# Kernel tuning notes

Measured on AMD Instinct MI355X. Metric: run time of the kernel, lower is better.

Reference implementation:

```python
import jax, jax.numpy as jnp
import numpy as np

Q_MAX = 127.0  # int8 symmetric quant range


def setup_inputs() -> dict:
    key = jax.random.key(0)
    kx, kw, ks = jax.random.split(key, 3)
    M, K, N = 16384, 4096, 4096
    x = jax.random.normal(kx, (M, K), dtype=jnp.float32)
    # int8 weight values in [-127, 127]
    weight = jax.random.randint(kw, (N, K), -127, 128, dtype=jnp.int32).astype(jnp.int8)
    # per-output-row dequant scale, small positive values as a real quantizer would produce
    weight_scale = jax.random.uniform(ks, (N, 1), dtype=jnp.float32, minval=1e-3, maxval=1e-2)
    return {"x": x, "weight": weight, "weight_scale": weight_scale}


def reference(x, weight, weight_scale):
    # --- per-token dynamic activation quantization (get_hip_quant(per_Token)) ---
    amax = jnp.max(jnp.abs(x), axis=-1, keepdims=True)            # [M,1]
    x_scale = amax / Q_MAX                                        # [M,1]
    x_q = jnp.clip(jnp.round(x / jnp.maximum(x_scale, 1e-8)), -Q_MAX, Q_MAX)  # int8 values, kept fp32
    # --- gemm_a8w8: int8xint8 GEMM with fused dequant (row scale_a * col scale_b) ---
    acc = jnp.einsum('mk,nk->mn', x_q, weight.astype(jnp.float32),
                     preferred_element_type=jnp.float32)          # [M,N] int accumulation in fp32
    y = acc * x_scale * weight_scale.T                            # fused dequant scales
    return y  # fp32 stand-in for otype=bf16 output
```

## Files before the change

### kernel.cpp

```cpp
#include <hip/hip_runtime.h>
#include <stdint.h>

#define M_DIM 16384
#define N_DIM 4096
#define K_DIM 4096

#define BM 256
#define BN 256
#define BK 128
#define NT (K_DIM / BK)

typedef int i32x4 __attribute__((ext_vector_type(4)));

__device__ __forceinline__ void async16(const uint8_t* g, uint8_t* l) {
    __builtin_amdgcn_global_load_lds(
        (const __attribute__((address_space(1))) void*)g,
        (__attribute__((address_space(3))) void*)l,
        16, 0, 0);
}

__global__ __launch_bounds__(256) void pack_w_kernel(const int* __restrict__ w32,
                                                     uint32_t* __restrict__ w8,
                                                     int n4) {
    int i = blockIdx.x * 256 + threadIdx.x;
    if (i < n4) {
        const int4 v = reinterpret_cast<const int4*>(w32)[i];
        uint32_t p = (uint32_t)(v.x & 255) | ((uint32_t)(v.y & 255) << 8) |
                     ((uint32_t)(v.z & 255) << 16) | ((uint32_t)(v.w & 255) << 24);
        w8[i] = p;
    }
}

__global__ __launch_bounds__(256) void quant_kernel(const float* __restrict__ x,
                                                    uint32_t* __restrict__ xq,
                                                    float* __restrict__ xscale) {
    const int m = blockIdx.x;
    const int t = threadIdx.x;
    const float4* row = reinterpret_cast<const float4*>(x + (size_t)m * K_DIM);
    float4 v[4];
    float amax = 0.0f;
#pragma unroll
    for (int i = 0; i < 4; ++i) {
        v[i] = row[t + i * 256];
        amax = fmaxf(amax, fmaxf(fmaxf(fabsf(v[i].x), fabsf(v[i].y)),
                                 fmaxf(fabsf(v[i].z), fabsf(v[i].w))));
    }
#pragma unroll
    for (int off = 32; off > 0; off >>= 1) amax = fmaxf(amax, __shfl_xor(amax, off));
    __shared__ float smax[4];
    if ((t & 63) == 0) smax[t >> 6] = amax;
    __syncthreads();
    amax = fmaxf(fmaxf(smax[0], smax[1]), fmaxf(smax[2], smax[3]));
    const float scale = amax / 127.0f;
    const float s = fmaxf(scale, 1e-8f);
    if (t == 0) xscale[m] = scale;
    uint32_t* orow = xq + (size_t)m * (K_DIM / 4);
#pragma unroll
    for (int i = 0; i < 4; ++i) {
        int q0 = __float2int_rn(v[i].x / s);
        int q1 = __float2int_rn(v[i].y / s);
        int q2 = __float2int_rn(v[i].z / s);
        int q3 = __float2int_rn(v[i].w / s);
        q0 = max(-127, min(127, q0));
        q1 = max(-127, min(127, q1));
        q2 = max(-127, min(127, q2));
        q3 = max(-127, min(127, q3));
        uint32_t p = (uint32_t)(q0 & 255) | ((uint32_t)(q1 & 255) << 8) |
                     ((uint32_t)(q2 & 255) << 16) | ((uint32_t)(q3 & 255) << 24);
        orow[t + i * 256] = p;
    }
}

__global__ __launch_bounds__(512, 2) void gemm_kernel(
    const uint8_t* __restrict__ Aq, const float* __restrict__ ascale,
    const uint8_t* __restrict__ Bq, const float* __restrict__ wscale,
    float* __restrict__ out) {
    __shared__ uint8_t lds[4 * BM * BK];
    uint8_t* ldsA0 = lds;
    uint8_t* ldsA1 = lds + BM * BK;
    uint8_t* ldsB0 = lds + 2 * BM * BK;
    uint8_t* ldsB1 = lds + 3 * BM * BK;

    const int tid = threadIdx.x;
    const int lane = tid & 63;
    const int w = tid >> 6;
    const int wr = w >> 2;
    const int wc = w & 3;
    const int lr = lane & 15;
    const int lg = lane >> 4;

    const int bid = blockIdx.x;
    const int swz = (bid & 7) * (1024 / 8) + (bid >> 3);
    const size_t row0 = (size_t)(swz >> 4) * BM;
    const size_t col0 = (size_t)(swz & 15) * BN;
    const uint8_t* Ab = Aq + row0 * K_DIM;
    const uint8_t* Bb = Bq + col0 * K_DIM;

    i32x4 acc[8][4];
#pragma unroll
    for (int i = 0; i < 8; ++i)
#pragma unroll
        for (int j = 0; j < 4; ++j) acc[i][j] = (i32x4){0, 0, 0, 0};

#define STAGE_P(BASE, DST, KT)                                                   \
    do {                                                                         \
        _Pragma("unroll") for (int it_ = 0; it_ < 4; ++it_) {                    \
            const int idx_ = it_ * 512 + tid;                                    \
            const int m_ = idx_ >> 3, p_ = idx_ & 7;                             \
            async16((BASE) + (size_t)m_ * K_DIM + (KT) * BK +                    \
                        ((p_ ^ (m_ & 7)) << 4),                                  \
                    (DST) + (it_ * 512 + w * 64) * 16);                          \
        }                                                                        \
    } while (0)

#define READ_K(BUFA, BUFB, KK, F)                                                \
    do {                                                                         \
        _Pragma("unroll") for (int q_ = 0; q_ < 8; ++q_) {                       \
            const int r_ = wr * 128 + q_ * 16 + lr;                              \
            const int u_ = (KK) * 4 + lg;                                        \
            afk[F][q_] = *reinterpret_cast<const i32x4*>(                        \
                (BUFA) + r_ * BK + ((u_ ^ (r_ & 7)) << 4));                      \
        }                                                                        \
        _Pragma("unroll") for (int p_ = 0; p_ < 4; ++p_) {                       \
            const int r_ = wc * 64 + p_ * 16 + lr;                               \
            const int u_ = (KK) * 4 + lg;                                        \
            bfk[F][p_] = *reinterpret_cast<const i32x4*>(                        \
                (BUFB) + r_ * BK + ((u_ ^ (r_ & 7)) << 4));                      \
        }                                                                        \
    } while (0)

#define CLUSTER(F)                                                               \
    do {                                                                         \
        __builtin_amdgcn_s_setprio(1);                                           \
        _Pragma("unroll") for (int q_ = 0; q_ < 8; ++q_)                         \
        _Pragma("unroll") for (int p_ = 0; p_ < 4; ++p_)                         \
            acc[q_][p_] = __builtin_amdgcn_mfma_i32_16x16x64_i8(                 \
                afk[F][q_], bfk[F][p_], acc[q_][p_], 0, 0, 0);                   \
        __builtin_amdgcn_s_setprio(0);                                           \
    } while (0)

#define BAR __builtin_amdgcn_s_barrier()
#define VMCNT(N) asm volatile("s_waitcnt vmcnt(" #N ")" ::: "memory")
#define LGKM0                                              \
    do {                                                   \
        asm volatile("s_waitcnt lgkmcnt(0)" ::: "memory"); \
        __builtin_amdgcn_sched_barrier(0);                 \
    } while (0)

#define TILE_ONE(CA, CB, NA, NB, TB, TA2, KA, KB)                                \
    do {                                                                         \
        LGKM0;                                               \
        STAGE_P(Bb, NB, TB);               \
        READ_K(CA, CB, KB, 1);           \
        CLUSTER(0);                                                              \
        LGKM0;                                                     \
        VMCNT(0);                     \
        BAR;                           \
        STAGE_P(Ab, CA, TA2);               \
        READ_K(NA, NB, KA, 0);            \
        CLUSTER(1);                                                              \
    } while (0)

#define MAIN_LOOP(KA, KB)                                                        \
    do {                                                                         \
        READ_K(ldsA0, ldsB0, KA, 0);                                             \
        _Pragma("unroll 1") for (int it2 = 0; it2 < NT / 2; ++it2) {             \
            const int T = 2 * it2;                                               \
            const int Tp2 = (T + 2 < NT) ? T + 2 : NT - 1;                       \
            const int Tp3 = (T + 3 < NT) ? T + 3 : NT - 1;                       \
            TILE_ONE(ldsA0, ldsB0, ldsA1, ldsB1, T + 1, Tp2, KA, KB);            \
            TILE_ONE(ldsA1, ldsB1, ldsA0, ldsB0, Tp2, Tp3, KA, KB);              \
        }                                                                        \
    } while (0)

    i32x4 afk[2][8], bfk[2][4];

    STAGE_P(Ab, ldsA0, 0);
    STAGE_P(Bb, ldsB0, 0);
    STAGE_P(Ab, ldsA1, 1);
    VMCNT(4);
    BAR;

    if (wr == 0) {
        MAIN_LOOP(0, 1);
    } else {
        MAIN_LOOP(1, 0);
    }

    const float* asp = ascale + row0 + wr * 128;
    const float* wsp = wscale + col0 + wc * 64;
    float wsv[4];
#pragma unroll
    for (int nf = 0; nf < 4; ++nf) wsv[nf] = wsp[nf * 16 + lr];
    float* outBase = out + (row0 + wr * 128) * (size_t)N_DIM + col0 + wc * 64;
#pragma unroll
    for (int mf = 0; mf < 8; ++mf) {
#pragma unroll
        for (int j = 0; j < 4; ++j) {
            const int r = mf * 16 + lg * 4 + j;
            const float av = asp[r];
            float* orow = outBase + (size_t)r * N_DIM;
#pragma unroll
            for (int nf = 0; nf < 4; ++nf) {
                orow[nf * 16 + lr] = (float)acc[mf][nf][j] * av * wsv[nf];
            }
        }
    }
#undef STAGE_P
#undef READ_K
#undef CLUSTER
#undef TILE_ONE
#undef MAIN_LOOP
#undef BAR
#undef VMCNT
#undef LGKM0
}

extern "C" void kernel_launch(void* const* d_in, const int* in_sizes, int n_in,
                              void* d_out, int out_size, void* d_ws, size_t ws_size,
                              hipStream_t stream) {
    const float* x = (const float*)d_in[0];
    const int* w32 = (const int*)d_in[1];
    const float* wscale = (const float*)d_in[2];
    float* out = (float*)d_out;

    uint8_t* ws = (uint8_t*)d_ws;
    uint32_t* xq = (uint32_t*)ws;
    float* xscale = (float*)(ws + (size_t)M_DIM * K_DIM);
    uint8_t* wq = ws + (size_t)M_DIM * K_DIM + (size_t)M_DIM * 4;

    pack_w_kernel<<<dim3((N_DIM * K_DIM / 4 + 255) / 256), 256, 0, stream>>>(
        w32, (uint32_t*)wq, N_DIM * K_DIM / 4);
    quant_kernel<<<dim3(M_DIM), 256, 0, stream>>>(x, xq, xscale);
    gemm_kernel<<<dim3((M_DIM / BM) * (N_DIM / BN)), 512, 0, stream>>>(
        (const uint8_t*)xq, xscale, wq, wscale, out);
}
```

Baseline: 343.8 us.

## Merge prep kernels, precompute LDS/global offsets, and unify GEMM staging schedule

Combines the weight-packing and activation-quantization kernels into a single launch, with extra blocks handling the weight pack. In the GEMM it precomputes the swizzled global and LDS offsets once per thread instead of per tile. It also replaces the per-wave-row split K-order main loop with a single loop that prefetches both A and B tiles two ahead, staging both after the barrier. This aims to cut address arithmetic and launch overhead, at the cost of more live registers and less staggered LDS traffic between wave rows.

```diff
diff --git a/kernel.cpp b/kernel.cpp
--- a/kernel.cpp
+++ b/kernel.cpp
@@ -19,23 +19,21 @@
         16, 0, 0);
 }
 
-__global__ __launch_bounds__(256) void pack_w_kernel(const int* __restrict__ w32,
-                                                     uint32_t* __restrict__ w8,
-                                                     int n4) {
-    int i = blockIdx.x * 256 + threadIdx.x;
-    if (i < n4) {
+__global__ __launch_bounds__(256) void prep_kernel(const float* __restrict__ x,
+                                                   const int* __restrict__ w32,
+                                                   uint32_t* __restrict__ xq,
+                                                   float* __restrict__ xscale,
+                                                   uint32_t* __restrict__ w8) {
+    const int b = blockIdx.x;
+    const int t = threadIdx.x;
+    if (b >= M_DIM) {
+        const int i = (b - M_DIM) * 256 + t;
         const int4 v = reinterpret_cast<const int4*>(w32)[i];
-        uint32_t p = (uint32_t)(v.x & 255) | ((uint32_t)(v.y & 255) << 8) |
-                     ((uint32_t)(v.z & 255) << 16) | ((uint32_t)(v.w & 255) << 24);
-        w8[i] = p;
-    }
-}
-
-__global__ __launch_bounds__(256) void quant_kernel(const float* __restrict__ x,
-                                                    uint32_t* __restrict__ xq,
-                                                    float* __restrict__ xscale) {
-    const int m = blockIdx.x;
-    const int t = threadIdx.x;
+        w8[i] = (uint32_t)(v.x & 255) | ((uint32_t)(v.y & 255) << 8) |
+                ((uint32_t)(v.z & 255) << 16) | ((uint32_t)(v.w & 255) << 24);
+        return;
+    }
+    const int m = b;
     const float4* row = reinterpret_cast<const float4*>(x + (size_t)m * K_DIM);
     float4 v[4];
     float amax = 0.0f;
@@ -65,9 +63,8 @@
         q1 = max(-127, min(127, q1));
         q2 = max(-127, min(127, q2));
         q3 = max(-127, min(127, q3));
-        uint32_t p = (uint32_t)(q0 & 255) | ((uint32_t)(q1 & 255) << 8) |
-                     ((uint32_t)(q2 & 255) << 16) | ((uint32_t)(q3 & 255) << 24);
-        orow[t + i * 256] = p;
+        orow[t + i * 256] = (uint32_t)(q0 & 255) | ((uint32_t)(q1 & 255) << 8) |
+                            ((uint32_t)(q2 & 255) << 16) | ((uint32_t)(q3 & 255) << 24);
     }
 }
 
@@ -96,37 +93,51 @@
     const uint8_t* Ab = Aq + row0 * K_DIM;
     const uint8_t* Bb = Bq + col0 * K_DIM;
 
+    int sgOff[4];
+#pragma unroll
+    for (int it = 0; it < 4; ++it) {
+        const int idx = it * 512 + tid;
+        const int m_ = idx >> 3, p_ = idx & 7;
+        sgOff[it] = m_ * K_DIM + ((p_ ^ (m_ & 7)) << 4);
+    }
+    int slOff[4];
+#pragma unroll
+    for (int it = 0; it < 4; ++it) slOff[it] = (it * 512 + w * 64) * 16;
+    int aRd[2][8], bRd[2][4];
+#pragma unroll
+    for (int kk = 0; kk < 2; ++kk) {
+#pragma unroll
+        for (int q = 0; q < 8; ++q) {
+            const int r = wr * 128 + q * 16 + lr;
+            const int u = kk * 4 + lg;
+            aRd[kk][q] = r * BK + ((u ^ (r & 7)) << 4);
+        }
+#pragma unroll
+        for (int p = 0; p < 4; ++p) {
+            const int r = wc * 64 + p * 16 + lr;
+            const int u = kk * 4 + lg;
+            bRd[kk][p] = r * BK + ((u ^ (r & 7)) << 4);
+        }
+    }
+
     i32x4 acc[8][4];
 #pragma unroll
     for (int i = 0; i < 8; ++i)
 #pragma unroll
         for (int j = 0; j < 4; ++j) acc[i][j] = (i32x4){0, 0, 0, 0};
 
-#define STAGE_P(BASE, DST, KT)                                                   \
-    do {                                                                         \
-        _Pragma("unroll") for (int it_ = 0; it_ < 4; ++it_) {                    \
-            const int idx_ = it_ * 512 + tid;                                    \
-            const int m_ = idx_ >> 3, p_ = idx_ & 7;                             \
-            async16((BASE) + (size_t)m_ * K_DIM + (KT) * BK +                    \
-                        ((p_ ^ (m_ & 7)) << 4),                                  \
-                    (DST) + (it_ * 512 + w * 64) * 16);                          \
-        }                                                                        \
+#define STAGE_P(BASE, DST, KOFF)                                                 \
+    do {                                                                         \
+        _Pragma("unroll") for (int it_ = 0; it_ < 4; ++it_)                      \
+            async16((BASE) + (size_t)(sgOff[it_] + (KOFF)), (DST) + slOff[it_]); \
     } while (0)
 
 #define READ_K(BUFA, BUFB, KK, F)                                                \
     do {                                                                         \
-        _Pragma("unroll") for (int q_ = 0; q_ < 8; ++q_) {                       \
-            const int r_ = wr * 128 + q_ * 16 + lr;                              \
-            const int u_ = (KK) * 4 + lg;                                        \
-            afk[F][q_] = *reinterpret_cast<const i32x4*>(                        \
-                (BUFA) + r_ * BK + ((u_ ^ (r_ & 7)) << 4));                      \
-        }                                                                        \
-        _Pragma("unroll") for (int p_ = 0; p_ < 4; ++p_) {                       \
-            const int r_ = wc * 64 + p_ * 16 + lr;                               \
-            const int u_ = (KK) * 4 + lg;                                        \
-            bfk[F][p_] = *reinterpret_cast<const i32x4*>(                        \
-                (BUFB) + r_ * BK + ((u_ ^ (r_ & 7)) << 4));                      \
-        }                                                                        \
+        _Pragma("unroll") for (int q_ = 0; q_ < 8; ++q_)                         \
+            afk[F][q_] = *reinterpret_cast<const i32x4*>((BUFA) + aRd[KK][q_]);  \
+        _Pragma("unroll") for (int p_ = 0; p_ < 4; ++p_)                         \
+            bfk[F][p_] = *reinterpret_cast<const i32x4*>((BUFB) + bRd[KK][p_]);  \
     } while (0)
 
 #define CLUSTER(F)                                                               \
@@ -147,44 +158,38 @@
         __builtin_amdgcn_sched_barrier(0);                 \
     } while (0)
 
-#define TILE_ONE(CA, CB, NA, NB, TB, TA2, KA, KB)                                \
-    do {                                                                         \
-        LGKM0;                                               \
-        STAGE_P(Bb, NB, TB);               \
-        READ_K(CA, CB, KB, 1);           \
+#define TILE_ONE(CA, CB, NA, NB, KOFF2)                                          \
+    do {                                                                         \
+        LGKM0;                               \
+        READ_K(CA, CB, 1, 1);                     \
         CLUSTER(0);                                                              \
         LGKM0;                                                     \
-        VMCNT(0);                     \
-        BAR;                           \
-        STAGE_P(Ab, CA, TA2);               \
-        READ_K(NA, NB, KA, 0);            \
+        VMCNT(0);                       \
+        BAR;                                     \
+        STAGE_P(Ab, CA, KOFF2);                     \
+        STAGE_P(Bb, CB, KOFF2);                     \
+        READ_K(NA, NB, 0, 0);                \
         CLUSTER(1);                                                              \
-    } while (0)
-
-#define MAIN_LOOP(KA, KB)                                                        \
-    do {                                                                         \
-        READ_K(ldsA0, ldsB0, KA, 0);                                             \
-        _Pragma("unroll 1") for (int it2 = 0; it2 < NT / 2; ++it2) {             \
-            const int T = 2 * it2;                                               \
-            const int Tp2 = (T + 2 < NT) ? T + 2 : NT - 1;                       \
-            const int Tp3 = (T + 3 < NT) ? T + 3 : NT - 1;                       \
-            TILE_ONE(ldsA0, ldsB0, ldsA1, ldsB1, T + 1, Tp2, KA, KB);            \
-            TILE_ONE(ldsA1, ldsB1, ldsA0, ldsB0, Tp2, Tp3, KA, KB);              \
-        }                                                                        \
     } while (0)
 
     i32x4 afk[2][8], bfk[2][4];
 
     STAGE_P(Ab, ldsA0, 0);
     STAGE_P(Bb, ldsB0, 0);
-    STAGE_P(Ab, ldsA1, 1);
-    VMCNT(4);
+    STAGE_P(Ab, ldsA1, BK);
+    STAGE_P(Bb, ldsB1, BK);
+    VMCNT(8);
     BAR;
-
-    if (wr == 0) {
-        MAIN_LOOP(0, 1);
-    } else {
-        MAIN_LOOP(1, 0);
+    READ_K(ldsA0, ldsB0, 0, 0);
+
+#pragma unroll 1
+    for (int it2 = 0; it2 < NT / 2; ++it2) {
+        const int T = 2 * it2;
+        const int k2 = ((T + 2 < NT) ? T + 2 : NT - 1) * BK;
+        const int k3 = ((T + 3 < NT) ? T + 3 : NT - 1) * BK;
+
+        TILE_ONE(ldsA0, ldsB0, ldsA1, ldsB1, k2);
+        TILE_ONE(ldsA1, ldsB1, ldsA0, ldsB0, k3);
     }
 
     const float* asp = ascale + row0 + wr * 128;
@@ -210,7 +215,6 @@
 #undef READ_K
 #undef CLUSTER
 #undef TILE_ONE
-#undef MAIN_LOOP
 #undef BAR
 #undef VMCNT
 #undef LGKM0
@@ -229,9 +233,8 @@
     float* xscale = (float*)(ws + (size_t)M_DIM * K_DIM);
     uint8_t* wq = ws + (size_t)M_DIM * K_DIM + (size_t)M_DIM * 4;
 
-    pack_w_kernel<<<dim3((N_DIM * K_DIM / 4 + 255) / 256), 256, 0, stream>>>(
-        w32, (uint32_t*)wq, N_DIM * K_DIM / 4);
-    quant_kernel<<<dim3(M_DIM), 256, 0, stream>>>(x, xq, xscale);
+    prep_kernel<<<dim3(M_DIM + N_DIM * K_DIM / 4 / 256), 256, 0, stream>>>(
+        x, w32, xq, xscale, (uint32_t*)wq);
     gemm_kernel<<<dim3((M_DIM / BM) * (N_DIM / BN)), 512, 0, stream>>>(
         (const uint8_t*)xq, xscale, wq, wscale, out);
 }
```

After: 350.7 us. +2.0%, slower.
